# Kernel optimization log

Hardware: AMD Instinct MI355X
Metric: run time of the kernel (lower is better)

Reference implementation:

```python
import jax, jax.numpy as jnp
import numpy as np

N_EMBD = 1024
HEAD_SIZE = 128
BLOCK_SIZE = 2048
B, T = 8, 2048

def setup_inputs() -> dict:
    key = jax.random.key(0)
    kx, kq, kk, kv = jax.random.split(key, 4)
    x = jax.random.normal(kx, (B, T, N_EMBD), dtype=jnp.float32)
    # nn.Linear(n_embd, head_size, bias=False) weights: [head_size, n_embd]
    s = 1.0 / np.sqrt(N_EMBD)
    Wq = jax.random.uniform(kq, (HEAD_SIZE, N_EMBD), jnp.float32, -s, s)
    Wk = jax.random.uniform(kk, (HEAD_SIZE, N_EMBD), jnp.float32, -s, s)
    Wv = jax.random.uniform(kv, (HEAD_SIZE, N_EMBD), jnp.float32, -s, s)
    return {"x": x, "Wq": Wq, "Wk": Wk, "Wv": Wv}

def reference(x, Wq, Wk, Wv):
    # q,k,v: [B,T,H]
    q = jnp.einsum('btc,hc->bth', x, Wq)
    k = jnp.einsum('btc,hc->bth', x, Wk)
    v = jnp.einsum('btc,hc->bth', x, Wv)
    scale = k.shape[-1] ** -0.5
    wei = jnp.einsum('bth,bsh->bts', q, k) * scale  # [B,T,T]
    Tq = q.shape[1]
    causal = jnp.tril(jnp.ones((Tq, Tq), dtype=bool))
    wei = jnp.where(causal[None, :, :], wei, -jnp.inf)
    wei = jax.nn.softmax(wei, axis=-1)
    out = jnp.einsum('bts,bsh->bth', wei, v)  # [B,T,H]
    return out
```

## Files before the change

kernel.cpp:

```cpp
#include <hip/hip_runtime.h>

#define B_ 8
#define T_ 2048
#define C_ 1024
#define H_ 128
#define BT_ (B_ * T_)

typedef __attribute__((ext_vector_type(8))) short short8;
typedef __attribute__((ext_vector_type(4))) float f32x4;
typedef __attribute__((ext_vector_type(16))) float f32x16;
typedef unsigned short u16;

#define SSCALE 0.12753257708482632f

static __device__ __forceinline__ u16 f2bf(float f) {
    union { float f; unsigned u; } x; x.f = f;
    unsigned r = x.u + 0x7fffu + ((x.u >> 16) & 1u);
    return (u16)(r >> 16);
}

static __device__ __forceinline__ unsigned long long pack4bf(float a, float b, float c, float d) {
    return (unsigned long long)f2bf(a) |
           ((unsigned long long)f2bf(b) << 16) |
           ((unsigned long long)f2bf(c) << 32) |
           ((unsigned long long)f2bf(d) << 48);
}

static __device__ __forceinline__ unsigned cvtpk(float lo, float hi) {
    unsigned r;
    asm("v_cvt_pk_bf16_f32 %0, %1, %2" : "=v"(r) : "v"(lo), "v"(hi));
    return r;
}

static __device__ __forceinline__ void pl32swap(unsigned &a, unsigned &b) {
    asm volatile("v_permlane32_swap_b32 %0, %1" : "+v"(a), "+v"(b));
}
static __device__ __forceinline__ void pl32swapf(float &a, float &b) {
    asm volatile("v_permlane32_swap_b32 %0, %1" : "+v"(a), "+v"(b));
}

#define GLDS16(g, l)                                                            \
    __builtin_amdgcn_global_load_lds(                                           \
        (const __attribute__((address_space(1))) void*)(g),                     \
        (__attribute__((address_space(3))) void*)(l), 16, 0, 0)

__global__ __launch_bounds__(256) void wconv_kernel(
    const float* __restrict__ Wq, const float* __restrict__ Wk,
    const float* __restrict__ Wv, u16* __restrict__ wb)
{
    int t = blockIdx.x * 256 + threadIdx.x;
    int e = t * 8;
    const float* __restrict__ src = (e < 131072) ? Wq : (e < 262144 ? Wk : Wv);
    int off = e & 131071;
    float4 f0 = *(const float4*)&src[off];
    float4 f1 = *(const float4*)&src[off + 4];
    union { unsigned long long u[2]; uint4 v; } pk;
    pk.u[0] = pack4bf(f0.x, f0.y, f0.z, f0.w);
    pk.u[1] = pack4bf(f1.x, f1.y, f1.z, f1.w);
    *(uint4*)&wb[e] = pk.v;
}

__global__ __launch_bounds__(512) void proj_kernel(
    const float* __restrict__ x, const u16* __restrict__ wb,
    u16* __restrict__ qo, u16* __restrict__ ko, u16* __restrict__ vt)
{
    __shared__ union {
        struct { u16 a[2][64 * 64]; u16 w[2][384 * 64]; } s;
        u16 c[64 * 136];
    } lds;

    const int tid = threadIdx.x;
    const int lane = tid & 63;
    const int wid = tid >> 6;
    const int wr = wid >> 2;
    const int wc = wid & 3;
    const int m0 = blockIdx.x * 64;

    const int gr = lane >> 3, gc = lane & 7;

    float4 va[2];

    f32x4 acc[2][6];
    #pragma unroll
    for (int i = 0; i < 2; i++)
        #pragma unroll
        for (int j = 0; j < 6; j++) acc[i][j] = f32x4{0.f, 0.f, 0.f, 0.f};

    #pragma unroll
    for (int p = 0; p < 2; p++) {
        int idx = p * 512 + tid, r = idx >> 4, cc = (idx & 15) * 4;
        va[p] = *(const float4*)&x[(size_t)(m0 + r) * C_ + cc];
    }
    #pragma unroll
    for (int jj = 0; jj < 6; jj++) {
        int j = wid * 6 + jj;
        int row = j * 8 + gr;
        GLDS16(wb + (size_t)row * C_ + ((gc ^ gr) * 8),
               (char*)lds.s.w[0] + j * 1024);
    }
    #pragma unroll
    for (int p = 0; p < 2; p++) {
        int idx = p * 512 + tid, r = idx >> 4, cc = (idx & 15) * 4;
        int byte = (r * 128 + cc * 2) ^ ((r & 7) << 4);
        *(unsigned long long*)((char*)lds.s.a[0] + byte) =
            pack4bf(va[p].x, va[p].y, va[p].z, va[p].w);
    }
    asm volatile("s_waitcnt vmcnt(0) lgkmcnt(0)" ::: "memory");
    __builtin_amdgcn_s_barrier();

    for (int k = 0; k < 16; k++) {
        const int pb = k & 1;
        const bool pre = (k + 1 < 16);
        if (pre) {
            const int k0n = (k + 1) * 64;
            #pragma unroll
            for (int p = 0; p < 2; p++) {
                int idx = p * 512 + tid, r = idx >> 4, cc = (idx & 15) * 4;
                va[p] = *(const float4*)&x[(size_t)(m0 + r) * C_ + k0n + cc];
            }
            #pragma unroll
            for (int jj = 0; jj < 6; jj++) {
                int j = wid * 6 + jj;
                int row = j * 8 + gr;
                GLDS16(wb + (size_t)row * C_ + k0n + ((gc ^ gr) * 8),
                       (char*)lds.s.w[pb ^ 1] + j * 1024);
            }
        }

        #pragma unroll
        for (int ks = 0; ks < 2; ks++) {
            short8 af[2], bf[6];
            #pragma unroll
            for (int i = 0; i < 2; i++) {
                int row = wr * 32 + i * 16 + (lane & 15);
                int byte = (row * 128 + ks * 64 + (lane >> 4) * 16) ^ ((row & 7) << 4);
                af[i] = *(const short8*)((const char*)lds.s.a[pb] + byte);
            }
            #pragma unroll
            for (int j = 0; j < 6; j++) {
                int n = wc * 96 + j * 16 + (lane & 15);
                int byte = (n * 128 + ks * 64 + (lane >> 4) * 16) ^ ((n & 7) << 4);
                bf[j] = *(const short8*)((const char*)lds.s.w[pb] + byte);
            }
            #pragma unroll
            for (int i = 0; i < 2; i++)
                #pragma unroll
                for (int j = 0; j < 6; j++)
                    acc[i][j] = __builtin_amdgcn_mfma_f32_16x16x32_bf16(
                        af[i], bf[j], acc[i][j], 0, 0, 0);
        }

        if (pre) {
            #pragma unroll
            for (int p = 0; p < 2; p++) {
                int idx = p * 512 + tid, r = idx >> 4, cc = (idx & 15) * 4;
                int byte = (r * 128 + cc * 2) ^ ((r & 7) << 4);
                *(unsigned long long*)((char*)lds.s.a[pb ^ 1] + byte) =
                    pack4bf(va[p].x, va[p].y, va[p].z, va[p].w);
            }
        }
        asm volatile("s_waitcnt vmcnt(0) lgkmcnt(0)" ::: "memory");
        __builtin_amdgcn_s_barrier();
    }

    const int b = m0 / T_;
    const int tloc = m0 % T_;
    #pragma unroll
    for (int i = 0; i < 2; i++) {
        #pragma unroll
        for (int j = 0; j < 6; j++) {
            int n = wc * 96 + j * 16 + (lane & 15);
            int wdx = n >> 7;
            int rowb = wr * 32 + i * 16 + (lane >> 4) * 4;
            if (wdx < 2) {
                u16* __restrict__ dst = wdx ? ko : qo;
                int col = n & 127;
                #pragma unroll
                for (int r = 0; r < 4; r++)
                    dst[(size_t)(m0 + rowb + r) * H_ + col] = f2bf(acc[i][j][r]);
            } else {
                int h = n - 256;
                #pragma unroll
                for (int r = 0; r < 4; r++)
                    lds.c[(rowb + r) * 136 + h] = f2bf(acc[i][j][r]);
            }
        }
    }
    __syncthreads();
    #pragma unroll
    for (int p = 0; p < 2; p++) {
        int idx = p * 512 + tid;
        int h = idx >> 3, tg = idx & 7;
        u16 pk[8];
        #pragma unroll
        for (int jj = 0; jj < 8; jj++) pk[jj] = lds.c[(tg * 8 + jj) * 136 + h];
        *(short8*)&vt[((size_t)b * H_ + h) * T_ + tloc + tg * 8] = *(const short8*)pk;
    }
}

template<int S>
__global__ __launch_bounds__(256, 2) void attn32_kernel(
    const u16* __restrict__ q, const u16* __restrict__ k, const u16* __restrict__ vt,
    float* __restrict__ out, float* __restrict__ po, float* __restrict__ lp)
{
    __shared__ u16 kt[2][64 * 128];
    __shared__ u16 vtt[2][128 * 64];

    const int tid = threadIdx.x, lane = tid & 63, wid = tid >> 6;
    const int hi = lane >> 5, l31 = lane & 31;

    const int bid = blockIdx.x;
    int b, qt, p;
    if (S == 1)      { b = bid >> 4; qt = bid & 15; p = 0; }
    else if (S == 2) { b = bid >> 5; qt = bid & 15; p = (bid >> 4) & 1; }
    else             { b = bid >> 6; qt = bid & 15; p = (bid >> 4) & 3; }
    const int total = 2 * qt + 2;
    const int s0 = p * total / S, s1 = (p + 1) * total / S;
    const int qbase = qt * 128;
    const int qrow = qbase + wid * 32 + l31;

    short8 qf[8];
    #pragma unroll
    for (int ks = 0; ks < 8; ks++)
        qf[ks] = *(const short8*)&q[((size_t)b * T_ + qrow) * H_ + ks * 16 + hi * 8];

    f32x16 ot0, ot1, ot2, ot3;
    #pragma unroll
    for (int i = 0; i < 16; i++) { ot0[i] = 0.f; ot1[i] = 0.f; ot2[i] = 0.f; ot3[i] = 0.f; }
    float lsum = 0.f;

    const u16* __restrict__ kb = k + (size_t)b * T_ * H_;
    const u16* __restrict__ vb = vt + (size_t)b * H_ * T_;

    auto stage = [&](int s, int pbuf) {
        const int kvbase = s * 64;
        #pragma unroll
        for (int jj = 0; jj < 4; jj++) {
            int j = wid * 4 + jj;
            int r = j * 4 + (lane >> 4), c = lane & 15;
            GLDS16(kb + (size_t)(kvbase + r) * H_ + ((c ^ (r & 7)) * 8),
                   (char*)kt[pbuf] + j * 1024);
        }
        #pragma unroll
        for (int jj = 0; jj < 4; jj++) {
            int j = wid * 4 + jj;
            int h = j * 8 + (lane >> 3), c = lane & 7;
            GLDS16(vb + (size_t)h * T_ + kvbase + ((c ^ (h & 7)) * 8),
                   (char*)vtt[pbuf] + j * 1024);
        }
    };

    if (s0 < s1) {
        stage(s0, 0);
        asm volatile("s_waitcnt vmcnt(0)" ::: "memory");
        __builtin_amdgcn_s_barrier();
    }

    for (int s = s0; s < s1; s++) {
        const int pb = (s - s0) & 1;
        if (s + 1 < s1) stage(s + 1, pb ^ 1);
        const int kvbase = s * 64;
        const char* __restrict__ ktb = (const char*)kt[pb];
        const char* __restrict__ vtb = (const char*)vtt[pb];

        f32x16 sa0, sa1;
        #pragma unroll
        for (int i = 0; i < 16; i++) { sa0[i] = 0.f; sa1[i] = 0.f; }
        __builtin_amdgcn_s_setprio(1);
        #pragma unroll
        for (int ks = 0; ks < 8; ks++) {
            const int ch = ks * 2 + hi;
            const int r0 = l31, r1 = 32 + l31;
            short8 a0 = *(const short8*)(ktb + r0 * 256 + ((ch ^ (r0 & 7)) << 4));
            short8 a1 = *(const short8*)(ktb + r1 * 256 + ((ch ^ (r1 & 7)) << 4));
            sa0 = __builtin_amdgcn_mfma_f32_32x32x16_bf16(a0, qf[ks], sa0, 0, 0, 0);
            sa1 = __builtin_amdgcn_mfma_f32_32x32x16_bf16(a1, qf[ks], sa1, 0, 0, 0);
        }
        __builtin_amdgcn_s_setprio(0);

        const bool dm = (s >= 2 * qt);
        float pv0[16], pv1[16];
        #pragma unroll
        for (int r = 0; r < 16; r++) {
            const int crow = (r & 3) + 8 * (r >> 2) + 4 * hi;
            float e0 = exp2f(sa0[r] * SSCALE);
            float e1 = exp2f(sa1[r] * SSCALE);
            if (dm) {
                if (kvbase + crow > qrow) e0 = 0.f;
                if (kvbase + 32 + crow > qrow) e1 = 0.f;
            }
            pv0[r] = e0; pv1[r] = e1;
            lsum += e0 + e1;
        }

        unsigned u0[8], u1[8];
        #pragma unroll
        for (int j = 0; j < 8; j++) {
            u0[j] = cvtpk(pv0[2 * j], pv0[2 * j + 1]);
            u1[j] = cvtpk(pv1[2 * j], pv1[2 * j + 1]);
        }
        pl32swap(u0[0], u0[2]); pl32swap(u0[1], u0[3]);
        pl32swap(u0[4], u0[6]); pl32swap(u0[5], u0[7]);
        pl32swap(u1[0], u1[2]); pl32swap(u1[1], u1[3]);
        pl32swap(u1[4], u1[6]); pl32swap(u1[5], u1[7]);
        union PKU { unsigned w[4]; short8 v; };
        PKU f0, f1, f2, f3;
        f0.w[0] = u0[0]; f0.w[1] = u0[1]; f0.w[2] = u0[2]; f0.w[3] = u0[3];
        f1.w[0] = u0[4]; f1.w[1] = u0[5]; f1.w[2] = u0[6]; f1.w[3] = u0[7];
        f2.w[0] = u1[0]; f2.w[1] = u1[1]; f2.w[2] = u1[2]; f2.w[3] = u1[3];
        f3.w[0] = u1[4]; f3.w[1] = u1[5]; f3.w[2] = u1[6]; f3.w[3] = u1[7];

        __builtin_amdgcn_s_setprio(1);
#define PV_DT(OT, DT)                                                               \
        {                                                                           \
            const int d = DT * 32 + l31;                                            \
            const char* vrow = vtb + d * 128;                                       \
            const int sw = d & 7;                                                   \
            short8 va0 = *(const short8*)(vrow + (((0 + hi) ^ sw) << 4));           \
            short8 va1 = *(const short8*)(vrow + (((2 + hi) ^ sw) << 4));           \
            short8 va2 = *(const short8*)(vrow + (((4 + hi) ^ sw) << 4));           \
            short8 va3 = *(const short8*)(vrow + (((6 + hi) ^ sw) << 4));           \
            OT = __builtin_amdgcn_mfma_f32_32x32x16_bf16(va0, f0.v, OT, 0, 0, 0);   \
            OT = __builtin_amdgcn_mfma_f32_32x32x16_bf16(va1, f1.v, OT, 0, 0, 0);   \
            OT = __builtin_amdgcn_mfma_f32_32x32x16_bf16(va2, f2.v, OT, 0, 0, 0);   \
            OT = __builtin_amdgcn_mfma_f32_32x32x16_bf16(va3, f3.v, OT, 0, 0, 0);   \
        }
        PV_DT(ot0, 0) PV_DT(ot1, 1) PV_DT(ot2, 2) PV_DT(ot3, 3)
#undef PV_DT
        __builtin_amdgcn_s_setprio(0);

        asm volatile("s_waitcnt vmcnt(0)" ::: "memory");
        __builtin_amdgcn_s_barrier();
    }

    float la = lsum, lb = lsum;
    pl32swapf(la, lb);
    const float ltot = la + lb;

    float* __restrict__ dst = (S == 1 || p == 0) ? out : (po + (size_t)(p - 1) * BT_ * H_);
    const float rinv = (S == 1) ? (1.0f / ltot) : 1.0f;
    float* __restrict__ orow = &dst[((size_t)b * T_ + qrow) * H_];
#define WR_DT(OT, DT)                                                   \
    {                                                                   \
        _Pragma("unroll")                                               \
        for (int g = 0; g < 4; g++) {                                   \
            float4 w4;                                                  \
            w4.x = OT[4 * g + 0] * rinv; w4.y = OT[4 * g + 1] * rinv;   \
            w4.z = OT[4 * g + 2] * rinv; w4.w = OT[4 * g + 3] * rinv;   \
            *(float4*)&orow[DT * 32 + g * 8 + hi * 4] = w4;             \
        }                                                               \
    }
    WR_DT(ot0, 0) WR_DT(ot1, 1) WR_DT(ot2, 2) WR_DT(ot3, 3)
#undef WR_DT
    if (S > 1 && lane < 32)
        lp[(size_t)p * BT_ + b * T_ + qrow] = ltot;
}

template<int S>
__global__ __launch_bounds__(256) void combineS_kernel(
    float* __restrict__ out, const float* __restrict__ po, const float* __restrict__ lp)
{
    int i = blockIdx.x * 256 + threadIdx.x;
    int row = i >> 5;
    float lt = lp[row];
    #pragma unroll
    for (int pp = 1; pp < S; pp++) lt += lp[(size_t)pp * BT_ + row];
    float inv = 1.0f / lt;
    float4 a = ((const float4*)out)[i];
    #pragma unroll
    for (int pp = 1; pp < S; pp++) {
        float4 c = ((const float4*)(po + (size_t)(pp - 1) * BT_ * H_))[i];
        a.x += c.x; a.y += c.y; a.z += c.z; a.w += c.w;
    }
    a.x *= inv; a.y *= inv; a.z *= inv; a.w *= inv;
    ((float4*)out)[i] = a;
}

extern "C" void kernel_launch(void* const* d_in, const int* in_sizes, int n_in,
                              void* d_out, int out_size, void* d_ws, size_t ws_size,
                              hipStream_t stream) {
    const float* x  = (const float*)d_in[0];
    const float* Wq = (const float*)d_in[1];
    const float* Wk = (const float*)d_in[2];
    const float* Wv = (const float*)d_in[3];

    u16* q  = (u16*)d_ws;
    u16* kk = q + (size_t)BT_ * H_;
    u16* vt = kk + (size_t)BT_ * H_;
    u16* wb = vt + (size_t)BT_ * H_;
    const size_t po_off = (size_t)3 * BT_ * H_ * 2 + 393216 * 2;
    float* po = (float*)((char*)d_ws + po_off);
    const size_t obytes = (size_t)BT_ * H_ * 4;
    const size_t need4 = po_off + 3 * obytes + (size_t)4 * BT_ * 4;
    const size_t need2 = po_off + 1 * obytes + (size_t)2 * BT_ * 4;

    wconv_kernel<<<192, 256, 0, stream>>>(Wq, Wk, Wv, wb);
    proj_kernel<<<256, 512, 0, stream>>>(x, wb, q, kk, vt);

    if (ws_size >= need4) {
        float* lpx = (float*)((char*)d_ws + po_off + 3 * obytes);
        attn32_kernel<4><<<512, 256, 0, stream>>>(q, kk, vt, (float*)d_out, po, lpx);
        combineS_kernel<4><<<2048, 256, 0, stream>>>((float*)d_out, po, lpx);
    } else if (ws_size >= need2) {
        float* lpx = (float*)((char*)d_ws + po_off + 1 * obytes);
        attn32_kernel<2><<<256, 256, 0, stream>>>(q, kk, vt, (float*)d_out, po, lpx);
        combineS_kernel<2><<<2048, 256, 0, stream>>>((float*)d_out, po, lpx);
    } else {
        attn32_kernel<1><<<128, 256, 0, stream>>>(q, kk, vt, (float*)d_out, nullptr, nullptr);
    }
}
```

Before: 157.2 us.

## Fold softmax scale into Wq and deepen x prefetch pipeline in projection

The softmax scale (log2e/sqrt(H)) is now folded into the bf16 Wq conversion, so the attention loop drops one multiply per score element before exp2. The projection kernel keeps three register slots of x prefetches, loading three k-tiles ahead with partial vmcnt waits instead of draining all loads every iteration, and fully unrolls the k loop. This is meant to hide global load latency in the projection, at the cost of more VGPRs and bf16 rounding of q after scaling, which may shift accuracy slightly.

```diff
diff --git a/kernel.cpp b/kernel.cpp
--- a/kernel.cpp
+++ b/kernel.cpp
@@ -51,12 +51,13 @@
     int t = blockIdx.x * 256 + threadIdx.x;
     int e = t * 8;
     const float* __restrict__ src = (e < 131072) ? Wq : (e < 262144 ? Wk : Wv);
+    const float sc = (e < 131072) ? SSCALE : 1.0f;
     int off = e & 131071;
     float4 f0 = *(const float4*)&src[off];
     float4 f1 = *(const float4*)&src[off + 4];
     union { unsigned long long u[2]; uint4 v; } pk;
-    pk.u[0] = pack4bf(f0.x, f0.y, f0.z, f0.w);
-    pk.u[1] = pack4bf(f1.x, f1.y, f1.z, f1.w);
+    pk.u[0] = pack4bf(f0.x * sc, f0.y * sc, f0.z * sc, f0.w * sc);
+    pk.u[1] = pack4bf(f1.x * sc, f1.y * sc, f1.z * sc, f1.w * sc);
     *(uint4*)&wb[e] = pk.v;
 }
 
@@ -78,7 +79,7 @@
 
     const int gr = lane >> 3, gc = lane & 7;
 
-    float4 va[2];
+    float4 va0[2], va1[2], va2[2];
 
     f32x4 acc[2][6];
     #pragma unroll
@@ -86,45 +87,53 @@
         #pragma unroll
         for (int j = 0; j < 6; j++) acc[i][j] = f32x4{0.f, 0.f, 0.f, 0.f};
 
-    #pragma unroll
-    for (int p = 0; p < 2; p++) {
-        int idx = p * 512 + tid, r = idx >> 4, cc = (idx & 15) * 4;
-        va[p] = *(const float4*)&x[(size_t)(m0 + r) * C_ + cc];
-    }
-    #pragma unroll
-    for (int jj = 0; jj < 6; jj++) {
-        int j = wid * 6 + jj;
-        int row = j * 8 + gr;
-        GLDS16(wb + (size_t)row * C_ + ((gc ^ gr) * 8),
-               (char*)lds.s.w[0] + j * 1024);
-    }
-    #pragma unroll
-    for (int p = 0; p < 2; p++) {
-        int idx = p * 512 + tid, r = idx >> 4, cc = (idx & 15) * 4;
-        int byte = (r * 128 + cc * 2) ^ ((r & 7) << 4);
-        *(unsigned long long*)((char*)lds.s.a[0] + byte) =
-            pack4bf(va[p].x, va[p].y, va[p].z, va[p].w);
-    }
-    asm volatile("s_waitcnt vmcnt(0) lgkmcnt(0)" ::: "memory");
+#define ALOAD(slot, kt)                                                          \
+    {                                                                            \
+        _Pragma("unroll")                                                        \
+        for (int p = 0; p < 2; p++) {                                            \
+            int idx = p * 512 + tid, r = idx >> 4, cc = (idx & 15) * 4;          \
+            slot[p] = *(const float4*)&x[(size_t)(m0 + r) * C_ + (kt) * 64 + cc];\
+        }                                                                        \
+    }
+#define AWRITE(slot, buf)                                                        \
+    {                                                                            \
+        _Pragma("unroll")                                                        \
+        for (int p = 0; p < 2; p++) {                                            \
+            int idx = p * 512 + tid, r = idx >> 4, cc = (idx & 15) * 4;          \
+            int byte = (r * 128 + cc * 2) ^ ((r & 7) << 4);                      \
+            *(unsigned long long*)((char*)lds.s.a[buf] + byte) =                 \
+                pack4bf(slot[p].x, slot[p].y, slot[p].z, slot[p].w);             \
+        }                                                                        \
+    }
+#define WISSUE(kt, buf)                                                          \
+    {                                                                            \
+        _Pragma("unroll")                                                        \
+        for (int jj = 0; jj < 6; jj++) {                                         \
+            int j = wid * 6 + jj;                                                \
+            int row = j * 8 + gr;                                                \
+            GLDS16(wb + (size_t)row * C_ + (kt) * 64 + ((gc ^ gr) * 8),          \
+                   (char*)lds.s.w[buf] + j * 1024);                              \
+        }                                                                        \
+    }
+
+    ALOAD(va0, 0)
+    AWRITE(va0, 0)
+    WISSUE(0, 0)
+    __builtin_amdgcn_sched_barrier(0);
+    ALOAD(va1, 1)
+    ALOAD(va2, 2)
+    asm volatile("s_waitcnt vmcnt(4) lgkmcnt(0)" ::: "memory");
     __builtin_amdgcn_s_barrier();
 
+    #pragma unroll
     for (int k = 0; k < 16; k++) {
         const int pb = k & 1;
-        const bool pre = (k + 1 < 16);
-        if (pre) {
-            const int k0n = (k + 1) * 64;
-            #pragma unroll
-            for (int p = 0; p < 2; p++) {
-                int idx = p * 512 + tid, r = idx >> 4, cc = (idx & 15) * 4;
-                va[p] = *(const float4*)&x[(size_t)(m0 + r) * C_ + k0n + cc];
-            }
-            #pragma unroll
-            for (int jj = 0; jj < 6; jj++) {
-                int j = wid * 6 + jj;
-                int row = j * 8 + gr;
-                GLDS16(wb + (size_t)row * C_ + k0n + ((gc ^ gr) * 8),
-                       (char*)lds.s.w[pb ^ 1] + j * 1024);
-            }
+        if (k + 1 <= 15) WISSUE(k + 1, pb ^ 1)
+        __builtin_amdgcn_sched_barrier(0);
+        if (k + 3 <= 15) {
+            if ((k % 3) == 0) ALOAD(va0, k + 3)
+            else if ((k % 3) == 1) ALOAD(va1, k + 3)
+            else ALOAD(va2, k + 3)
         }
 
         #pragma unroll
@@ -150,18 +159,19 @@
                         af[i], bf[j], acc[i][j], 0, 0, 0);
         }
 
-        if (pre) {
-            #pragma unroll
-            for (int p = 0; p < 2; p++) {
-                int idx = p * 512 + tid, r = idx >> 4, cc = (idx & 15) * 4;
-                int byte = (r * 128 + cc * 2) ^ ((r & 7) << 4);
-                *(unsigned long long*)((char*)lds.s.a[pb ^ 1] + byte) =
-                    pack4bf(va[p].x, va[p].y, va[p].z, va[p].w);
-            }
-        }
-        asm volatile("s_waitcnt vmcnt(0) lgkmcnt(0)" ::: "memory");
+        if (k + 1 <= 15) {
+            if (((k + 1) % 3) == 0) AWRITE(va0, pb ^ 1)
+            else if (((k + 1) % 3) == 1) AWRITE(va1, pb ^ 1)
+            else AWRITE(va2, pb ^ 1)
+        }
+
+        if (k <= 12)      asm volatile("s_waitcnt vmcnt(2) lgkmcnt(0)" ::: "memory");
+        else              asm volatile("s_waitcnt vmcnt(0) lgkmcnt(0)" ::: "memory");
         __builtin_amdgcn_s_barrier();
     }
+#undef ALOAD
+#undef AWRITE
+#undef WISSUE
 
     const int b = m0 / T_;
     const int tloc = m0 % T_;
@@ -279,25 +289,24 @@
         __builtin_amdgcn_s_setprio(0);
 
         const bool dm = (s >= 2 * qt);
-        float pv0[16], pv1[16];
         #pragma unroll
         for (int r = 0; r < 16; r++) {
             const int crow = (r & 3) + 8 * (r >> 2) + 4 * hi;
-            float e0 = exp2f(sa0[r] * SSCALE);
-            float e1 = exp2f(sa1[r] * SSCALE);
+            float e0 = exp2f(sa0[r]);
+            float e1 = exp2f(sa1[r]);
             if (dm) {
                 if (kvbase + crow > qrow) e0 = 0.f;
                 if (kvbase + 32 + crow > qrow) e1 = 0.f;
             }
-            pv0[r] = e0; pv1[r] = e1;
+            sa0[r] = e0; sa1[r] = e1;
             lsum += e0 + e1;
         }
 
         unsigned u0[8], u1[8];
         #pragma unroll
         for (int j = 0; j < 8; j++) {
-            u0[j] = cvtpk(pv0[2 * j], pv0[2 * j + 1]);
-            u1[j] = cvtpk(pv1[2 * j], pv1[2 * j + 1]);
+            u0[j] = cvtpk(sa0[2 * j], sa0[2 * j + 1]);
+            u1[j] = cvtpk(sa1[2 * j], sa1[2 * j + 1]);
         }
         pl32swap(u0[0], u0[2]); pl32swap(u0[1], u0[3]);
         pl32swap(u0[4], u0[6]); pl32swap(u0[5], u0[7]);
```

Measured after the change: 154.1 us. 1.02x faster.
